# Kernel optimization log

Measured on AMD Instinct MI355X. Metric: run time of the kernel, lower is better.

## Reference

```python
import jax, jax.numpy as jnp
import numpy as np

N1, N2, N3 = 40000, 30000, 30000
N = N1 + N2 + N3          # total nodes after vstack
E = 800000                # edges
D_IN = 256                # in_channels
D_HID = 256               # 2 * out_channels
D_OUT = 128               # out_channels


def _glorot(k, shape):
    lim = (6.0 / (shape[0] + shape[1])) ** 0.5
    return jax.random.uniform(k, shape, jnp.float32, -lim, lim)


def setup_inputs() -> dict:
    key = jax.random.key(0)
    ks = jax.random.split(key, 12)
    x1 = jax.random.normal(ks[0], (N1, 128), jnp.float32)
    x2 = jax.random.normal(ks[1], (N2, 256), jnp.float32)
    x3 = jax.random.normal(ks[2], (N3, 64), jnp.float32)
    edge_index = jax.random.randint(ks[3], (2, E), 0, N, jnp.int64)
    return {
        "x1": x1, "x2": x2, "x3": x3,
        "Wp1": _glorot(ks[4], (128, D_IN)), "bp1": jnp.zeros((D_IN,), jnp.float32),
        "Wp2": _glorot(ks[5], (256, D_IN)), "bp2": jnp.zeros((D_IN,), jnp.float32),
        "Wp3": _glorot(ks[6], (64, D_IN)),  "bp3": jnp.zeros((D_IN,), jnp.float32),
        "W1": _glorot(ks[7], (D_IN, D_HID)), "b1": jnp.zeros((D_HID,), jnp.float32),
        "W2": _glorot(ks[8], (D_HID, D_OUT)), "b2": jnp.zeros((D_OUT,), jnp.float32),
        "edge_index": edge_index,
    }


def _gcn_conv(x, W, b, src, dst, dis):
    # PyG GCNConv: h = xW; out[j] = sum_i norm_ij * h[i] (incl. self-loop) + b
    h = x @ W                                   # [N, d_out]
    msg = h[src] * (dis[src] * dis[dst])[:, None]   # [E, d_out] edge messages
    agg = jax.ops.segment_sum(msg, dst, num_segments=N)
    agg = agg + h * (dis * dis)[:, None]        # self-loop term (norm = 1/deg)
    return agg + b


def reference(x1, x2, x3, Wp1, bp1, Wp2, bp2, Wp3, bp3, W1, b1, W2, b2, edge_index):
    # per-type projection + vstack
    x = jnp.concatenate([x1 @ Wp1 + bp1, x2 @ Wp2 + bp2, x3 @ Wp3 + bp3], axis=0)
    # dropout(p=0.5) is identity in eval mode (deterministic baseline)
    src, dst = edge_index[0], edge_index[1]
    # degree with self-loops (in-degree at dst, as in PyG gcn_norm)
    deg = jnp.ones((N,), x.dtype).at[dst].add(1.0)
    dis = jax.lax.rsqrt(deg)                    # deg^{-1/2}
    h = jax.nn.relu(_gcn_conv(x, W1, b1, src, dst, dis))
    return _gcn_conv(h, W2, b2, src, dst, dis)
```

## Files before the change

### kernel.cpp

```cpp
#include <hip/hip_runtime.h>
#include <cstddef>

#define NT 100000
#define NN1 40000
#define NN2 30000
#define NN3 30000
#define EE 800000

typedef _Float16 f16;
typedef f16 f16x8 __attribute__((ext_vector_type(8)));
typedef f16 f16x4 __attribute__((ext_vector_type(4)));
typedef float f32x4 __attribute__((ext_vector_type(4)));

static inline int cdiv(int a, int b) { return (a + b - 1) / b; }

__device__ __forceinline__ void gload_lds16(const f16* g, f16* l) {
    __builtin_amdgcn_global_load_lds(
        (const __attribute__((address_space(1))) void*)g,
        (__attribute__((address_space(3))) void*)l, 16, 0, 0);
}

__global__ void k_hist(const int* __restrict__ dst, int* __restrict__ cnt, int e) {
    int i = blockIdx.x * blockDim.x + threadIdx.x;
    if (i < e) atomicAdd(&cnt[dst[i]], 1);
}

__global__ void k_scan1(const int* __restrict__ cnt, int* __restrict__ rowptr,
                        int* __restrict__ part, float* __restrict__ dis, int n) {
    __shared__ int sums[256];
    int b = blockIdx.x, t = threadIdx.x;
    int base = b * 1024 + t * 4;
    int v0 = (base + 0 < n) ? cnt[base + 0] : 0;
    int v1 = (base + 1 < n) ? cnt[base + 1] : 0;
    int v2 = (base + 2 < n) ? cnt[base + 2] : 0;
    int v3 = (base + 3 < n) ? cnt[base + 3] : 0;
    if (base + 0 < n) dis[base + 0] = rsqrtf((float)v0 + 1.0f);
    if (base + 1 < n) dis[base + 1] = rsqrtf((float)v1 + 1.0f);
    if (base + 2 < n) dis[base + 2] = rsqrtf((float)v2 + 1.0f);
    if (base + 3 < n) dis[base + 3] = rsqrtf((float)v3 + 1.0f);
    int tsum = v0 + v1 + v2 + v3;
    sums[t] = tsum;
    __syncthreads();
    for (int off = 1; off < 256; off <<= 1) {
        int y = (t >= off) ? sums[t - off] : 0;
        __syncthreads();
        sums[t] += y;
        __syncthreads();
    }
    int excl = sums[t] - tsum;
    if (base + 0 < n) rowptr[base + 0] = excl;
    if (base + 1 < n) rowptr[base + 1] = excl + v0;
    if (base + 2 < n) rowptr[base + 2] = excl + v0 + v1;
    if (base + 3 < n) rowptr[base + 3] = excl + v0 + v1 + v2;
    if (t == 255) part[b] = sums[255];
}

__global__ void k_scan2(int* __restrict__ part, int nb) {
    __shared__ int sums[256];
    int t = threadIdx.x;
    int v = (t < nb) ? part[t] : 0;
    sums[t] = v;
    __syncthreads();
    for (int off = 1; off < 256; off <<= 1) {
        int y = (t >= off) ? sums[t - off] : 0;
        __syncthreads();
        sums[t] += y;
        __syncthreads();
    }
    if (t < nb) part[t] = sums[t] - v;
}

__global__ void k_scan3(int* __restrict__ rowptr, const int* __restrict__ part,
                        int n, int total) {
    int i = blockIdx.x * blockDim.x + threadIdx.x;
    if (i < n) rowptr[i] += part[i >> 10];
    if (i == 0) rowptr[n] = total;
}

__global__ void k_fill(const int* __restrict__ src, const int* __restrict__ dst,
                       const float* __restrict__ dis, const int* __restrict__ rowptr,
                       int* __restrict__ cursor, int2* __restrict__ e_pairs, int e) {
    int i = blockIdx.x * blockDim.x + threadIdx.x;
    if (i >= e) return;
    int s = src[i], t = dst[i];
    int pos = atomicAdd(&cursor[t], 1);
    int2 p;
    p.x = s;
    p.y = __float_as_int(dis[s] * dis[t]);
    e_pairs[rowptr[t] + pos] = p;
}

__global__ void k_cvt_all(const float* __restrict__ a, int na4,
                          const float* __restrict__ b, int nb4,
                          const float* __restrict__ c, int nc4,
                          f16* __restrict__ o) {
    int i = blockIdx.x * blockDim.x + threadIdx.x;
    const float* s; int j;
    if (i < na4) { s = a; j = i; }
    else if (i < na4 + nb4) { s = b; j = i - na4; }
    else if (i < na4 + nb4 + nc4) { s = c; j = i - na4 - nb4; }
    else return;
    float4 v = reinterpret_cast<const float4*>(s)[j];
    f16x4 r = {(f16)v.x, (f16)v.y, (f16)v.z, (f16)v.w};
    reinterpret_cast<f16x4*>(o)[i] = r;
}

struct TArgs {
    const float *W0, *W1, *W2, *W3, *W4;
    f16 *T0, *T1, *T2, *T3, *T4;
};
__global__ void k_transpose_all(TArgs t) {
    int i = blockIdx.x * blockDim.x + threadIdx.x;
    const float* W; f16* T; int K, N, j;
    if      (i <  32768) { W = t.W0; T = t.T0; K = 128; N = 256; j = i; }
    else if (i <  98304) { W = t.W1; T = t.T1; K = 256; N = 256; j = i - 32768; }
    else if (i < 114688) { W = t.W2; T = t.T2; K =  64; N = 256; j = i - 98304; }
    else if (i < 180224) { W = t.W3; T = t.T3; K = 256; N = 256; j = i - 114688; }
    else if (i < 212992) { W = t.W4; T = t.T4; K = 256; N = 128; j = i - 180224; }
    else return;
    int k = j / N, n = j - k * N;
    T[n * K + k] = (f16)W[j];
}

template<bool RELU_OUT, bool HAS_BIAS>
__device__ __forceinline__
void hgemm_body(f16* As, f16* Bs,
                const f16* __restrict__ A, const f16* __restrict__ BT,
                const float* __restrict__ bias, f16* __restrict__ C,
                int M, int K, int N, int bx, int by) {
    const int tid = threadIdx.x;
    const int lane = tid & 63;
    const int wid = tid >> 6;
    const int wm = wid & 1, wn = wid >> 1;
    const int bm = bx * 128;
    const int bn = by * 128;
    const int r15 = lane & 15, g = lane >> 4;
    const int sr  = lane >> 2;
    const int chs = (lane & 3) ^ ((lane >> 3) & 3);

    auto stage = [&](int buf, int k0) {
        #pragma unroll
        for (int q = 0; q < 2; ++q) {
            int chunk = wid + q * 4;
            int row = chunk * 16 + sr;
            int ga = bm + row; if (ga >= M) ga = M - 1;
            gload_lds16(A  + (size_t)ga * K + k0 + chs * 8, As + buf * 4096 + chunk * 512);
            gload_lds16(BT + (size_t)(bn + row) * K + k0 + chs * 8, Bs + buf * 4096 + chunk * 512);
        }
    };

    f32x4 acc[4][4] = {};
    const int nsteps = K >> 5;
    stage(0, 0);
    __syncthreads();
    int cur = 0;
    for (int step = 0; step < nsteps; ++step) {
        if (step + 1 < nsteps) stage(cur ^ 1, (step + 1) << 5);
        f16x8 af[4], bf[4];
        const int sl = (g ^ ((r15 >> 1) & 3)) * 8;
        #pragma unroll
        for (int mf = 0; mf < 4; ++mf) {
            int row = wm * 64 + mf * 16 + r15;
            af[mf] = *reinterpret_cast<const f16x8*>(As + cur * 4096 + row * 32 + sl);
        }
        #pragma unroll
        for (int nf = 0; nf < 4; ++nf) {
            int row = wn * 64 + nf * 16 + r15;
            bf[nf] = *reinterpret_cast<const f16x8*>(Bs + cur * 4096 + row * 32 + sl);
        }
        #pragma unroll
        for (int mf = 0; mf < 4; ++mf)
            #pragma unroll
            for (int nf = 0; nf < 4; ++nf)
                acc[mf][nf] = __builtin_amdgcn_mfma_f32_16x16x32_f16(af[mf], bf[nf], acc[mf][nf], 0, 0, 0);
        __syncthreads();
        cur ^= 1;
    }

    #pragma unroll
    for (int mf = 0; mf < 4; ++mf) {
        #pragma unroll
        for (int nf = 0; nf < 4; ++nf) {
            int col = bn + wn * 64 + nf * 16 + r15;
            float bv = HAS_BIAS ? bias[col] : 0.f;
            #pragma unroll
            for (int r = 0; r < 4; ++r) {
                int rowg = bm + wm * 64 + mf * 16 + g * 4 + r;
                if (rowg < M) {
                    float v = acc[mf][nf][r] + bv;
                    if (RELU_OUT) v = fmaxf(v, 0.f);
                    C[(size_t)rowg * N + col] = (f16)v;
                }
            }
        }
    }
}

struct P3 {
    const f16 *a1, *a2, *a3, *t1, *t2, *t3;
    const float *b1, *b2, *b3;
    f16 *o1, *o2, *o3;
    int g1, g2;
};
__global__ __launch_bounds__(256) void k_proj3(P3 p) {
    extern __shared__ f16 smem[];
    int bx = blockIdx.x, by = blockIdx.y;
    if (bx < p.g1)
        hgemm_body<false, true>(smem, smem + 8192, p.a1, p.t1, p.b1, p.o1, NN1, 128, 256, bx, by);
    else if (bx < p.g1 + p.g2)
        hgemm_body<false, true>(smem, smem + 8192, p.a2, p.t2, p.b2, p.o2, NN2, 256, 256, bx - p.g1, by);
    else
        hgemm_body<false, true>(smem, smem + 8192, p.a3, p.t3, p.b3, p.o3, NN3, 64, 256, bx - p.g1 - p.g2, by);
}

__global__ __launch_bounds__(512)
void k_fused(const f16* __restrict__ x16, const float* __restrict__ dis,
             const int* __restrict__ rowptr, const int2* __restrict__ e_pairs,
             const f16* __restrict__ W1T, const float* __restrict__ b1,
             const f16* __restrict__ W2T, f16* __restrict__ hw2, int M) {
    __shared__ f16 P[64 * 256];
    const int tid = threadIdx.x;
    const int lane = tid & 63;
    const int bm = blockIdx.x * 64;

    {
        const int grp = tid >> 5;
        const int l = tid & 31;
        #pragma unroll
        for (int it = 0; it < 4; ++it) {
            int row = it * 16 + grp;
            int node = bm + row;
            float av[8];
            if (node < M) {
                float dj = dis[node];
                int r0 = rowptr[node], r1 = rowptr[node + 1];
                int deg = r1 - r0;
                int si = 0; float wi = 0.f;
                if (l < deg) { int2 pr = e_pairs[r0 + l]; si = pr.x; wi = __int_as_float(pr.y); }
                f16x8 a = reinterpret_cast<const f16x8*>(x16 + (size_t)node * 256)[l];
                float wself = dj * dj;
                #pragma unroll
                for (int k = 0; k < 8; ++k) av[k] = (float)a[k] * wself;
                int n32 = deg < 32 ? deg : 32;
                int e = 0;
                for (; e + 4 <= n32; e += 4) {
                    int s0 = __shfl(si, e + 0, 32), s1 = __shfl(si, e + 1, 32);
                    int s2 = __shfl(si, e + 2, 32), s3 = __shfl(si, e + 3, 32);
                    float w0 = __shfl(wi, e + 0, 32), w1 = __shfl(wi, e + 1, 32);
                    float w2 = __shfl(wi, e + 2, 32), w3 = __shfl(wi, e + 3, 32);
                    f16x8 u0 = reinterpret_cast<const f16x8*>(x16 + (size_t)s0 * 256)[l];
                    f16x8 u1 = reinterpret_cast<const f16x8*>(x16 + (size_t)s1 * 256)[l];
                    f16x8 u2 = reinterpret_cast<const f16x8*>(x16 + (size_t)s2 * 256)[l];
                    f16x8 u3 = reinterpret_cast<const f16x8*>(x16 + (size_t)s3 * 256)[l];
                    #pragma unroll
                    for (int k = 0; k < 8; ++k)
                        av[k] += (float)u0[k] * w0 + (float)u1[k] * w1
                               + (float)u2[k] * w2 + (float)u3[k] * w3;
                }
                for (; e < n32; ++e) {
                    int s0 = __shfl(si, e, 32);
                    float w0 = __shfl(wi, e, 32);
                    f16x8 u0 = reinterpret_cast<const f16x8*>(x16 + (size_t)s0 * 256)[l];
                    #pragma unroll
                    for (int k = 0; k < 8; ++k) av[k] += (float)u0[k] * w0;
                }
                for (int e2 = r0 + 32; e2 < r1; ++e2) {
                    int2 pr = e_pairs[e2];
                    float w0 = __int_as_float(pr.y);
                    f16x8 u0 = reinterpret_cast<const f16x8*>(x16 + (size_t)pr.x * 256)[l];
                    #pragma unroll
                    for (int k = 0; k < 8; ++k) av[k] += (float)u0[k] * w0;
                }
            } else {
                #pragma unroll
                for (int k = 0; k < 8; ++k) av[k] = 0.f;
            }
            f16x8 r;
            #pragma unroll
            for (int k = 0; k < 8; ++k) r[k] = (f16)av[k];
            int slot = (l & 3) ^ ((row >> 1) & 3);
            *reinterpret_cast<f16x8*>(P + (l >> 2) * 2048 + row * 32 + slot * 8) = r;
        }
    }
    __syncthreads();

    const int w = tid >> 6;
    const int r15 = lane & 15, g = lane >> 4;
    f32x4 acc[4][2] = {};
    for (int step = 0; step < 8; ++step) {
        f16x8 af[4], bf[2];
        #pragma unroll
        for (int mf = 0; mf < 4; ++mf) {
            int row = mf * 16 + r15;
            int slot = g ^ ((row >> 1) & 3);
            af[mf] = *reinterpret_cast<const f16x8*>(P + step * 2048 + row * 32 + slot * 8);
        }
        #pragma unroll
        for (int nf = 0; nf < 2; ++nf) {
            int n1 = w * 32 + nf * 16 + r15;
            bf[nf] = *reinterpret_cast<const f16x8*>(W1T + (size_t)n1 * 256 + step * 32 + g * 8);
        }
        #pragma unroll
        for (int mf = 0; mf < 4; ++mf)
            #pragma unroll
            for (int nf = 0; nf < 2; ++nf)
                acc[mf][nf] = __builtin_amdgcn_mfma_f32_16x16x32_f16(af[mf], bf[nf], acc[mf][nf], 0, 0, 0);
    }
    __syncthreads();

    #pragma unroll
    for (int nf = 0; nf < 2; ++nf) {
        int col = w * 32 + nf * 16 + r15;
        float bv = b1[col];
        int gp = (col >> 3) & 3, c7 = col & 7;
        #pragma unroll
        for (int mf = 0; mf < 4; ++mf) {
            #pragma unroll
            for (int rr = 0; rr < 4; ++rr) {
                int row = mf * 16 + g * 4 + rr;
                float v = fmaxf(acc[mf][nf][rr] + bv, 0.f);
                int slot = gp ^ ((row >> 1) & 3);
                P[w * 2048 + row * 32 + slot * 8 + c7] = (f16)v;
            }
        }
    }
    __syncthreads();

    f32x4 acc2[4] = {};
    for (int step = 0; step < 8; ++step) {
        f16x8 af[4], bf;
        #pragma unroll
        for (int mf = 0; mf < 4; ++mf) {
            int row = mf * 16 + r15;
            int slot = g ^ ((row >> 1) & 3);
            af[mf] = *reinterpret_cast<const f16x8*>(P + step * 2048 + row * 32 + slot * 8);
        }
        int n2 = w * 16 + r15;
        bf = *reinterpret_cast<const f16x8*>(W2T + (size_t)n2 * 256 + step * 32 + g * 8);
        #pragma unroll
        for (int mf = 0; mf < 4; ++mf)
            acc2[mf] = __builtin_amdgcn_mfma_f32_16x16x32_f16(af[mf], bf, acc2[mf], 0, 0, 0);
    }

    #pragma unroll
    for (int mf = 0; mf < 4; ++mf) {
        int col = w * 16 + r15;
        #pragma unroll
        for (int rr = 0; rr < 4; ++rr) {
            int rowg = bm + mf * 16 + g * 4 + rr;
            if (rowg < M)
                hw2[(size_t)rowg * 128 + col] = (f16)acc2[mf][rr];
        }
    }
}

__global__ void k_gather128(const f16* __restrict__ f, const float* __restrict__ dis,
                            const int* __restrict__ rowptr, const int2* __restrict__ e_pairs,
                            const float* __restrict__ bias, float* __restrict__ outb, int n) {
    int node = (int)(((long long)blockIdx.x * blockDim.x + threadIdx.x) >> 5);
    int l = threadIdx.x & 31;
    if (node >= n) return;
    float dj = dis[node];
    int r0 = rowptr[node], r1 = rowptr[node + 1];
    int deg = r1 - r0;
    int si = 0; float wi = 0.f;
    if (l < deg) { int2 p = e_pairs[r0 + l]; si = p.x; wi = __int_as_float(p.y); }
    f16x4 a = reinterpret_cast<const f16x4*>(f + (size_t)node * 128)[l];
    float wsf = dj * dj;
    float acc[4];
    #pragma unroll
    for (int k = 0; k < 4; ++k) acc[k] = (float)a[k] * wsf;
    int n32 = deg < 32 ? deg : 32;
    int e = 0;
    for (; e + 4 <= n32; e += 4) {
        int s0 = __shfl(si, e + 0, 32), s1 = __shfl(si, e + 1, 32);
        int s2 = __shfl(si, e + 2, 32), s3 = __shfl(si, e + 3, 32);
        float w0 = __shfl(wi, e + 0, 32), w1 = __shfl(wi, e + 1, 32);
        float w2 = __shfl(wi, e + 2, 32), w3 = __shfl(wi, e + 3, 32);
        f16x4 u0 = reinterpret_cast<const f16x4*>(f + (size_t)s0 * 128)[l];
        f16x4 u1 = reinterpret_cast<const f16x4*>(f + (size_t)s1 * 128)[l];
        f16x4 u2 = reinterpret_cast<const f16x4*>(f + (size_t)s2 * 128)[l];
        f16x4 u3 = reinterpret_cast<const f16x4*>(f + (size_t)s3 * 128)[l];
        #pragma unroll
        for (int k = 0; k < 4; ++k)
            acc[k] += (float)u0[k] * w0 + (float)u1[k] * w1 + (float)u2[k] * w2 + (float)u3[k] * w3;
    }
    for (; e < n32; ++e) {
        int s0 = __shfl(si, e, 32);
        float w0 = __shfl(wi, e, 32);
        f16x4 u0 = reinterpret_cast<const f16x4*>(f + (size_t)s0 * 128)[l];
        #pragma unroll
        for (int k = 0; k < 4; ++k) acc[k] += (float)u0[k] * w0;
    }
    for (int e2 = r0 + 32; e2 < r1; ++e2) {
        int2 p = e_pairs[e2];
        float w0 = __int_as_float(p.y);
        f16x4 u0 = reinterpret_cast<const f16x4*>(f + (size_t)p.x * 128)[l];
        #pragma unroll
        for (int k = 0; k < 4; ++k) acc[k] += (float)u0[k] * w0;
    }
    float4 bb = reinterpret_cast<const float4*>(bias)[l];
    float4 r = make_float4(acc[0] + bb.x, acc[1] + bb.y, acc[2] + bb.z, acc[3] + bb.w);
    reinterpret_cast<float4*>(outb + (size_t)node * 128)[l] = r;
}

extern "C" void kernel_launch(void* const* d_in, const int* in_sizes, int n_in,
                              void* d_out, int out_size, void* d_ws, size_t ws_size,
                              hipStream_t stream) {
    const float* x1  = (const float*)d_in[0];
    const float* x2  = (const float*)d_in[1];
    const float* x3  = (const float*)d_in[2];
    const float* Wp1 = (const float*)d_in[3];
    const float* bp1 = (const float*)d_in[4];
    const float* Wp2 = (const float*)d_in[5];
    const float* bp2 = (const float*)d_in[6];
    const float* Wp3 = (const float*)d_in[7];
    const float* bp3 = (const float*)d_in[8];
    const float* W1  = (const float*)d_in[9];
    const float* b1  = (const float*)d_in[10];
    const float* W2  = (const float*)d_in[11];
    const float* b2  = (const float*)d_in[12];
    const int*   ei  = (const int*)d_in[13];
    const int* src = ei;
    const int* dst = ei + EE;
    float* out = (float*)d_out;

    char* ws = (char*)d_ws;
    size_t off = 0;
    auto alloc = [&](size_t bytes) {
        char* p = ws + off;
        off += (bytes + 511) & ~(size_t)511;
        return p;
    };
    float* dis    = (float*)alloc((size_t)NT * 4);
    int*   cnt    = (int*)alloc((size_t)NT * 4);
    int*   cursor = (int*)alloc((size_t)NT * 4);
    int*   rowptr = (int*)alloc((size_t)(NT + 1) * 4);
    int*   part   = (int*)alloc(256 * 4);
    int2*  e_pairs= (int2*)alloc((size_t)EE * 8);
    f16*   x16    = (f16*)alloc((size_t)NT * 256 * 2);
    f16*   hw216  = (f16*)alloc((size_t)NT * 128 * 2);
    f16*   xc     = (f16*)alloc((size_t)(NN1 * 128 + NN2 * 256 + NN3 * 64) * 2);
    f16*   Wp1T   = (f16*)alloc((size_t)256 * 128 * 2);
    f16*   Wp2T   = (f16*)alloc((size_t)256 * 256 * 2);
    f16*   Wp3T   = (f16*)alloc((size_t)256 * 64 * 2);
    f16*   W1T    = (f16*)alloc((size_t)256 * 256 * 2);
    f16*   W2T    = (f16*)alloc((size_t)128 * 256 * 2);

    f16* x1c = xc;
    f16* x2c = xc + (size_t)NN1 * 128;
    f16* x3c = xc + (size_t)NN1 * 128 + (size_t)NN2 * 256;

    const int nb = cdiv(NT, 1024);

    size_t zspan = (size_t)((char*)rowptr - (char*)cnt);
    hipMemsetAsync(cnt, 0, zspan, stream);
    k_hist<<<cdiv(EE, 256), 256, 0, stream>>>(dst, cnt, EE);
    k_scan1<<<nb, 256, 0, stream>>>(cnt, rowptr, part, dis, NT);
    k_scan2<<<1, 256, 0, stream>>>(part, nb);
    k_scan3<<<cdiv(NT, 256), 256, 0, stream>>>(rowptr, part, NT, EE);
    k_fill<<<cdiv(EE, 256), 256, 0, stream>>>(src, dst, dis, rowptr, cursor, e_pairs, EE);

    {
        int na4 = NN1 * 128 / 4, nb4 = NN2 * 256 / 4, nc4 = NN3 * 64 / 4;
        k_cvt_all<<<cdiv(na4 + nb4 + nc4, 256), 256, 0, stream>>>(x1, na4, x2, nb4, x3, nc4, xc);
        TArgs t = {Wp1, Wp2, Wp3, W1, W2, Wp1T, Wp2T, Wp3T, W1T, W2T};
        k_transpose_all<<<cdiv(212992, 256), 256, 0, stream>>>(t);
    }

    {
        P3 p = {x1c, x2c, x3c, Wp1T, Wp2T, Wp3T, bp1, bp2, bp3,
                x16, x16 + (size_t)NN1 * 256, x16 + (size_t)(NN1 + NN2) * 256,
                cdiv(NN1, 128), cdiv(NN2, 128)};
        dim3 g(cdiv(NN1, 128) + cdiv(NN2, 128) + cdiv(NN3, 128), 2);
        k_proj3<<<g, 256, 32768, stream>>>(p);
    }

    k_fused<<<cdiv(NT, 64), 512, 0, stream>>>(x16, dis, rowptr, e_pairs,
                                              W1T, b1, W2T, hw216, NT);

    k_gather128<<<cdiv(NT * 32, 256), 256, 0, stream>>>(hw216, dis, rowptr, e_pairs, b2, out, NT);
}
```

Before: 287.6 us.

## Merge independent prep kernels into combined launches and widen gather unroll to 8

Combines the histogram, input fp16 conversion and weight transpose into one launch partitioned by block index. It also merges the CSR fill with the projection GEMM, so the two can share the GPU instead of running back to back. Separately, the neighbour gather loops in the fused layer-1 kernel and the final gather kernel now issue 8 independent row loads per step instead of 4, for more memory-level parallelism. The risks are higher register pressure and that the fill blocks now run with the 32 KB dynamic LDS reserved for the GEMM, which can lower their occupancy.

```diff
diff --git a/kernel.cpp b/kernel.cpp
--- a/kernel.cpp
+++ b/kernel.cpp
@@ -18,11 +18,6 @@
     __builtin_amdgcn_global_load_lds(
         (const __attribute__((address_space(1))) void*)g,
         (__attribute__((address_space(3))) void*)l, 16, 0, 0);
-}
-
-__global__ void k_hist(const int* __restrict__ dst, int* __restrict__ cnt, int e) {
-    int i = blockIdx.x * blockDim.x + threadIdx.x;
-    if (i < e) atomicAdd(&cnt[dst[i]], 1);
 }
 
 __global__ void k_scan1(const int* __restrict__ cnt, int* __restrict__ rowptr,
@@ -77,49 +72,48 @@
     if (i == 0) rowptr[n] = total;
 }
 
-__global__ void k_fill(const int* __restrict__ src, const int* __restrict__ dst,
-                       const float* __restrict__ dis, const int* __restrict__ rowptr,
-                       int* __restrict__ cursor, int2* __restrict__ e_pairs, int e) {
-    int i = blockIdx.x * blockDim.x + threadIdx.x;
-    if (i >= e) return;
-    int s = src[i], t = dst[i];
-    int pos = atomicAdd(&cursor[t], 1);
-    int2 p;
-    p.x = s;
-    p.y = __float_as_int(dis[s] * dis[t]);
-    e_pairs[rowptr[t] + pos] = p;
-}
-
-__global__ void k_cvt_all(const float* __restrict__ a, int na4,
-                          const float* __restrict__ b, int nb4,
-                          const float* __restrict__ c, int nc4,
-                          f16* __restrict__ o) {
-    int i = blockIdx.x * blockDim.x + threadIdx.x;
-    const float* s; int j;
-    if (i < na4) { s = a; j = i; }
-    else if (i < na4 + nb4) { s = b; j = i - na4; }
-    else if (i < na4 + nb4 + nc4) { s = c; j = i - na4 - nb4; }
-    else return;
-    float4 v = reinterpret_cast<const float4*>(s)[j];
-    f16x4 r = {(f16)v.x, (f16)v.y, (f16)v.z, (f16)v.w};
-    reinterpret_cast<f16x4*>(o)[i] = r;
-}
-
 struct TArgs {
     const float *W0, *W1, *W2, *W3, *W4;
     f16 *T0, *T1, *T2, *T3, *T4;
 };
-__global__ void k_transpose_all(TArgs t) {
-    int i = blockIdx.x * blockDim.x + threadIdx.x;
-    const float* W; f16* T; int K, N, j;
-    if      (i <  32768) { W = t.W0; T = t.T0; K = 128; N = 256; j = i; }
-    else if (i <  98304) { W = t.W1; T = t.T1; K = 256; N = 256; j = i - 32768; }
-    else if (i < 114688) { W = t.W2; T = t.T2; K =  64; N = 256; j = i - 98304; }
-    else if (i < 180224) { W = t.W3; T = t.T3; K = 256; N = 256; j = i - 114688; }
-    else if (i < 212992) { W = t.W4; T = t.T4; K = 256; N = 128; j = i - 180224; }
-    else return;
-    int k = j / N, n = j - k * N;
-    T[n * K + k] = (f16)W[j];
+#define HB   3125
+#define CVTB 14375
+#define TRB  832
+#define NA4  1280000
+#define NB4  1920000
+#define NC4  480000
+struct PrepArgs {
+    const int* dst; int* cnt;
+    const float *x1, *x2, *x3; f16* xc;
+    TArgs t;
+};
+__global__ __launch_bounds__(256) void k_prep(PrepArgs a) {
+    int bid = blockIdx.x, tid = threadIdx.x;
+    if (bid < HB) {
+        int i = bid * 256 + tid;
+        if (i < EE) atomicAdd(&a.cnt[a.dst[i]], 1);
+    } else if (bid < HB + CVTB) {
+        int i = (bid - HB) * 256 + tid;
+        const float* s; int j;
+        if (i < NA4) { s = a.x1; j = i; }
+        else if (i < NA4 + NB4) { s = a.x2; j = i - NA4; }
+        else if (i < NA4 + NB4 + NC4) { s = a.x3; j = i - NA4 - NB4; }
+        else return;
+        float4 v = reinterpret_cast<const float4*>(s)[j];
+        f16x4 r = {(f16)v.x, (f16)v.y, (f16)v.z, (f16)v.w};
+        reinterpret_cast<f16x4*>(a.xc)[i] = r;
+    } else {
+        int i = (bid - HB - CVTB) * 256 + tid;
+        const float* W; f16* T; int K, N, j;
+        if      (i <  32768) { W = a.t.W0; T = a.t.T0; K = 128; N = 256; j = i; }
+        else if (i <  98304) { W = a.t.W1; T = a.t.T1; K = 256; N = 256; j = i - 32768; }
+        else if (i < 114688) { W = a.t.W2; T = a.t.T2; K =  64; N = 256; j = i - 98304; }
+        else if (i < 180224) { W = a.t.W3; T = a.t.T3; K = 256; N = 256; j = i - 114688; }
+        else if (i < 212992) { W = a.t.W4; T = a.t.T4; K = 256; N = 128; j = i - 180224; }
+        else return;
+        int k = j / N, n = j - k * N;
+        T[n * K + k] = (f16)W[j];
+    }
 }
 
 template<bool RELU_OUT, bool HAS_BIAS>
@@ -202,15 +196,37 @@
     f16 *o1, *o2, *o3;
     int g1, g2;
 };
-__global__ __launch_bounds__(256) void k_proj3(P3 p) {
+#define FB 3125
+struct FPArgs {
+    const int *src, *dst;
+    const float* dis;
+    const int* rowptr;
+    int* cursor;
+    int2* e_pairs;
+    P3 p;
+};
+__global__ __launch_bounds__(256) void k_fillproj(FPArgs a) {
     extern __shared__ f16 smem[];
-    int bx = blockIdx.x, by = blockIdx.y;
-    if (bx < p.g1)
-        hgemm_body<false, true>(smem, smem + 8192, p.a1, p.t1, p.b1, p.o1, NN1, 128, 256, bx, by);
-    else if (bx < p.g1 + p.g2)
-        hgemm_body<false, true>(smem, smem + 8192, p.a2, p.t2, p.b2, p.o2, NN2, 256, 256, bx - p.g1, by);
-    else
-        hgemm_body<false, true>(smem, smem + 8192, p.a3, p.t3, p.b3, p.o3, NN3, 64, 256, bx - p.g1 - p.g2, by);
+    int bid = blockIdx.x;
+    if (bid < FB) {
+        int i = bid * 256 + threadIdx.x;
+        if (i >= EE) return;
+        int s = a.src[i], t = a.dst[i];
+        int pos = atomicAdd(&a.cursor[t], 1);
+        int2 pr;
+        pr.x = s;
+        pr.y = __float_as_int(a.dis[s] * a.dis[t]);
+        a.e_pairs[a.rowptr[t] + pos] = pr;
+    } else {
+        int pb = bid - FB;
+        int bx = pb >> 1, by = pb & 1;
+        if (bx < a.p.g1)
+            hgemm_body<false, true>(smem, smem + 8192, a.p.a1, a.p.t1, a.p.b1, a.p.o1, NN1, 128, 256, bx, by);
+        else if (bx < a.p.g1 + a.p.g2)
+            hgemm_body<false, true>(smem, smem + 8192, a.p.a2, a.p.t2, a.p.b2, a.p.o2, NN2, 256, 256, bx - a.p.g1, by);
+        else
+            hgemm_body<false, true>(smem, smem + 8192, a.p.a3, a.p.t3, a.p.b3, a.p.o3, NN3, 64, 256, bx - a.p.g1 - a.p.g2, by);
+    }
 }
 
 __global__ __launch_bounds__(512)
@@ -237,25 +253,43 @@
                 int deg = r1 - r0;
                 int si = 0; float wi = 0.f;
                 if (l < deg) { int2 pr = e_pairs[r0 + l]; si = pr.x; wi = __int_as_float(pr.y); }
-                f16x8 a = reinterpret_cast<const f16x8*>(x16 + (size_t)node * 256)[l];
+                f16x8 sa = reinterpret_cast<const f16x8*>(x16 + (size_t)node * 256)[l];
                 float wself = dj * dj;
                 #pragma unroll
-                for (int k = 0; k < 8; ++k) av[k] = (float)a[k] * wself;
+                for (int k = 0; k < 8; ++k) av[k] = (float)sa[k] * wself;
                 int n32 = deg < 32 ? deg : 32;
                 int e = 0;
+                for (; e + 8 <= n32; e += 8) {
+                    int s[8]; float w[8];
+                    #pragma unroll
+                    for (int q = 0; q < 8; ++q) {
+                        s[q] = __shfl(si, e + q, 32);
+                        w[q] = __shfl(wi, e + q, 32);
+                    }
+                    f16x8 u[8];
+                    #pragma unroll
+                    for (int q = 0; q < 8; ++q)
+                        u[q] = reinterpret_cast<const f16x8*>(x16 + (size_t)s[q] * 256)[l];
+                    #pragma unroll
+                    for (int q = 0; q < 8; ++q)
+                        #pragma unroll
+                        for (int k = 0; k < 8; ++k) av[k] += (float)u[q][k] * w[q];
+                }
                 for (; e + 4 <= n32; e += 4) {
-                    int s0 = __shfl(si, e + 0, 32), s1 = __shfl(si, e + 1, 32);
-                    int s2 = __shfl(si, e + 2, 32), s3 = __shfl(si, e + 3, 32);
-                    float w0 = __shfl(wi, e + 0, 32), w1 = __shfl(wi, e + 1, 32);
-                    float w2 = __shfl(wi, e + 2, 32), w3 = __shfl(wi, e + 3, 32);
-                    f16x8 u0 = reinterpret_cast<const f16x8*>(x16 + (size_t)s0 * 256)[l];
-                    f16x8 u1 = reinterpret_cast<const f16x8*>(x16 + (size_t)s1 * 256)[l];
-                    f16x8 u2 = reinterpret_cast<const f16x8*>(x16 + (size_t)s2 * 256)[l];
-                    f16x8 u3 = reinterpret_cast<const f16x8*>(x16 + (size_t)s3 * 256)[l];
-                    #pragma unroll
-                    for (int k = 0; k < 8; ++k)
-                        av[k] += (float)u0[k] * w0 + (float)u1[k] * w1
-                               + (float)u2[k] * w2 + (float)u3[k] * w3;
+                    int s[4]; float w[4];
+                    #pragma unroll
+                    for (int q = 0; q < 4; ++q) {
+                        s[q] = __shfl(si, e + q, 32);
+                        w[q] = __shfl(wi, e + q, 32);
+                    }
+                    f16x8 u[4];
+                    #pragma unroll
+                    for (int q = 0; q < 4; ++q)
+                        u[q] = reinterpret_cast<const f16x8*>(x16 + (size_t)s[q] * 256)[l];
+                    #pragma unroll
+                    for (int q = 0; q < 4; ++q)
+                        #pragma unroll
+                        for (int k = 0; k < 8; ++k) av[k] += (float)u[q][k] * w[q];
                 }
                 for (; e < n32; ++e) {
                     int s0 = __shfl(si, e, 32);
@@ -372,18 +406,37 @@
     for (int k = 0; k < 4; ++k) acc[k] = (float)a[k] * wsf;
     int n32 = deg < 32 ? deg : 32;
     int e = 0;
+    for (; e + 8 <= n32; e += 8) {
+        int s[8]; float w[8];
+        #pragma unroll
+        for (int q = 0; q < 8; ++q) {
+            s[q] = __shfl(si, e + q, 32);
+            w[q] = __shfl(wi, e + q, 32);
+        }
+        f16x4 u[8];
+        #pragma unroll
+        for (int q = 0; q < 8; ++q)
+            u[q] = reinterpret_cast<const f16x4*>(f + (size_t)s[q] * 128)[l];
+        #pragma unroll
+        for (int q = 0; q < 8; ++q)
+            #pragma unroll
+            for (int k = 0; k < 4; ++k) acc[k] += (float)u[q][k] * w[q];
+    }
     for (; e + 4 <= n32; e += 4) {
-        int s0 = __shfl(si, e + 0, 32), s1 = __shfl(si, e + 1, 32);
-        int s2 = __shfl(si, e + 2, 32), s3 = __shfl(si, e + 3, 32);
-        float w0 = __shfl(wi, e + 0, 32), w1 = __shfl(wi, e + 1, 32);
-        float w2 = __shfl(wi, e + 2, 32), w3 = __shfl(wi, e + 3, 32);
-        f16x4 u0 = reinterpret_cast<const f16x4*>(f + (size_t)s0 * 128)[l];
-        f16x4 u1 = reinterpret_cast<const f16x4*>(f + (size_t)s1 * 128)[l];
-        f16x4 u2 = reinterpret_cast<const f16x4*>(f + (size_t)s2 * 128)[l];
-        f16x4 u3 = reinterpret_cast<const f16x4*>(f + (size_t)s3 * 128)[l];
-        #pragma unroll
-        for (int k = 0; k < 4; ++k)
-            acc[k] += (float)u0[k] * w0 + (float)u1[k] * w1 + (float)u2[k] * w2 + (float)u3[k] * w3;
+        int s[4]; float w[4];
+        #pragma unroll
+        for (int q = 0; q < 4; ++q) {
+            s[q] = __shfl(si, e + q, 32);
+            w[q] = __shfl(wi, e + q, 32);
+        }
+        f16x4 u[4];
+        #pragma unroll
+        for (int q = 0; q < 4; ++q)
+            u[q] = reinterpret_cast<const f16x4*>(f + (size_t)s[q] * 128)[l];
+        #pragma unroll
+        for (int q = 0; q < 4; ++q)
+            #pragma unroll
+            for (int k = 0; k < 4; ++k) acc[k] += (float)u[q][k] * w[q];
     }
     for (; e < n32; ++e) {
         int s0 = __shfl(si, e, 32);
@@ -455,25 +508,28 @@
 
     size_t zspan = (size_t)((char*)rowptr - (char*)cnt);
     hipMemsetAsync(cnt, 0, zspan, stream);
-    k_hist<<<cdiv(EE, 256), 256, 0, stream>>>(dst, cnt, EE);
+
+    {
+        PrepArgs a;
+        a.dst = dst; a.cnt = cnt;
+        a.x1 = x1; a.x2 = x2; a.x3 = x3; a.xc = xc;
+        a.t = {Wp1, Wp2, Wp3, W1, W2, Wp1T, Wp2T, Wp3T, W1T, W2T};
+        k_prep<<<HB + CVTB + TRB, 256, 0, stream>>>(a);
+    }
+
     k_scan1<<<nb, 256, 0, stream>>>(cnt, rowptr, part, dis, NT);
     k_scan2<<<1, 256, 0, stream>>>(part, nb);
     k_scan3<<<cdiv(NT, 256), 256, 0, stream>>>(rowptr, part, NT, EE);
-    k_fill<<<cdiv(EE, 256), 256, 0, stream>>>(src, dst, dis, rowptr, cursor, e_pairs, EE);
 
     {
-        int na4 = NN1 * 128 / 4, nb4 = NN2 * 256 / 4, nc4 = NN3 * 64 / 4;
-        k_cvt_all<<<cdiv(na4 + nb4 + nc4, 256), 256, 0, stream>>>(x1, na4, x2, nb4, x3, nc4, xc);
-        TArgs t = {Wp1, Wp2, Wp3, W1, W2, Wp1T, Wp2T, Wp3T, W1T, W2T};
-        k_transpose_all<<<cdiv(212992, 256), 256, 0, stream>>>(t);
-    }
-
-    {
-        P3 p = {x1c, x2c, x3c, Wp1T, Wp2T, Wp3T, bp1, bp2, bp3,
-                x16, x16 + (size_t)NN1 * 256, x16 + (size_t)(NN1 + NN2) * 256,
-                cdiv(NN1, 128), cdiv(NN2, 128)};
-        dim3 g(cdiv(NN1, 128) + cdiv(NN2, 128) + cdiv(NN3, 128), 2);
-        k_proj3<<<g, 256, 32768, stream>>>(p);
+        FPArgs a;
+        a.src = src; a.dst = dst; a.dis = dis; a.rowptr = rowptr;
+        a.cursor = cursor; a.e_pairs = e_pairs;
+        a.p = {x1c, x2c, x3c, Wp1T, Wp2T, Wp3T, bp1, bp2, bp3,
+               x16, x16 + (size_t)NN1 * 256, x16 + (size_t)(NN1 + NN2) * 256,
+               cdiv(NN1, 128), cdiv(NN2, 128)};
+        int projb = (cdiv(NN1, 128) + cdiv(NN2, 128) + cdiv(NN3, 128)) * 2;
+        k_fillproj<<<FB + projb, 256, 32768, stream>>>(a);
     }
 
     k_fused<<<cdiv(NT, 64), 512, 0, stream>>>(x16, dis, rowptr, e_pairs,
```

New measurement: 277.3 us. 3.6% less time.
